# Kernel tuning notes

Hardware: AMD Instinct MI355X
Metric: run time of the kernel (lower is better)

The kernel has to match this reference:

```python
import jax, jax.numpy as jnp
import numpy as np

SEQ, B, I, H = 2048, 64, 512, 512


def setup_inputs() -> dict:
    key = jax.random.key(0)
    ks = jax.random.split(key, 5)
    s = 1.0 / np.sqrt(H)  # torch.nn.RNN init scale
    return {
        "x": jax.random.normal(ks[0], (SEQ, B, I), dtype=jnp.float32),
        "W_ih": jax.random.normal(ks[1], (H, I), dtype=jnp.float32) * s,
        "W_hh": jax.random.normal(ks[2], (H, H), dtype=jnp.float32) * s,
        "b_ih": jax.random.normal(ks[3], (H,), dtype=jnp.float32) * s,
        "b_hh": jax.random.normal(ks[4], (H,), dtype=jnp.float32) * s,
    }


def reference(x, W_ih, W_hh, b_ih, b_hh):
    # Precompute input projection for all timesteps in one big GEMM: [T,B,H]
    xw = jnp.einsum("tbi,hi->tbh", x, W_ih) + b_ih + b_hh

    def step(h, xt):
        # h: [B,H]; xt: [B,H] (already includes x_t W_ih^T + biases)
        h = jnp.tanh(xt + h @ W_hh.T)
        return h, h

    h0 = jnp.zeros((x.shape[1], W_hh.shape[0]), dtype=x.dtype)
    _, out = jax.lax.scan(step, h0, xw)  # out: [T,B,H]
    return out.reshape(-1, W_hh.shape[0])  # [T*B, H], matches out.view(-1, hidden)
```

## Files before the change

### kernel.cpp

```cpp
#include <hip/hip_runtime.h>
#include <cmath>


#define SEQ_T 2048
#define BATCH 64
#define KDIM 512
#define HDIM 512

typedef __fp16 h2v __attribute__((ext_vector_type(2)));
typedef __fp16 f16x8 __attribute__((ext_vector_type(8)));
typedef float f32x4 __attribute__((ext_vector_type(4)));

static __device__ __forceinline__ f16x8 pk8(float4 a, float4 b) {
  h2v p0 = __builtin_amdgcn_cvt_pkrtz(a.x, a.y);
  h2v p1 = __builtin_amdgcn_cvt_pkrtz(a.z, a.w);
  h2v p2 = __builtin_amdgcn_cvt_pkrtz(b.x, b.y);
  h2v p3 = __builtin_amdgcn_cvt_pkrtz(b.z, b.w);
  f16x8 r;
  r[0] = p0[0]; r[1] = p0[1]; r[2] = p1[0]; r[3] = p1[1];
  r[4] = p2[0]; r[5] = p2[1]; r[6] = p3[0]; r[7] = p3[1];
  return r;
}

#define G_LDA 72

#define MFM(mt, nt) \
  d##mt##nt = __builtin_amdgcn_mfma_f32_16x16x32_f16(fa##mt, fb##nt, d##mt##nt, 0, 0, 0);

#define EPI(mt, nt, bb)                                                     \
  {                                                                         \
    int row = m0 + wm + mt * 16 + (l >> 4) * 4;                             \
    int col = n0 + wn + nt * 16 + (l & 15);                                 \
    out[(size_t)(row + 0) * HDIM + col] = d##mt##nt[0] + bb;                \
    out[(size_t)(row + 1) * HDIM + col] = d##mt##nt[1] + bb;                \
    out[(size_t)(row + 2) * HDIM + col] = d##mt##nt[2] + bb;                \
    out[(size_t)(row + 3) * HDIM + col] = d##mt##nt[3] + bb;                \
  }

__global__ __launch_bounds__(256) void xw_gemm(const float* __restrict__ x,
                                               const float* __restrict__ Wih,
                                               const float* __restrict__ bih,
                                               const float* __restrict__ bhh,
                                               float* __restrict__ out) {
  __shared__ __fp16 At[128 * G_LDA];
  __shared__ __fp16 Bt[64 * G_LDA];
  const int tid = threadIdx.x;
  const int l = tid & 63;
  const int w = tid >> 6;
  const int m0 = (blockIdx.x >> 3) * 128;
  const int n0 = (blockIdx.x & 7) * 64;
  const int wm = (w >> 1) * 64;
  const int wn = (w & 1) * 32;

  const float bias0 = bih[n0 + wn + (l & 15)] + bhh[n0 + wn + (l & 15)];
  const float bias1 = bih[n0 + wn + 16 + (l & 15)] + bhh[n0 + wn + 16 + (l & 15)];

  f32x4 d00 = {0,0,0,0}, d01 = {0,0,0,0}, d10 = {0,0,0,0}, d11 = {0,0,0,0};
  f32x4 d20 = {0,0,0,0}, d21 = {0,0,0,0}, d30 = {0,0,0,0}, d31 = {0,0,0,0};

  for (int k0 = 0; k0 < KDIM; k0 += 64) {
    __syncthreads();
#pragma unroll
    for (int p = 0; p < 4; ++p) {
      int idx = tid + p * 256;
      int r = idx >> 3, sg = idx & 7;
      const float* ps = x + (size_t)(m0 + r) * KDIM + k0 + sg * 8;
      *(f16x8*)(At + r * G_LDA + sg * 8) =
          pk8(*(const float4*)ps, *(const float4*)(ps + 4));
    }
#pragma unroll
    for (int p = 0; p < 2; ++p) {
      int idx = tid + p * 256;
      int r = idx >> 3, sg = idx & 7;
      const float* ps = Wih + (size_t)(n0 + r) * KDIM + k0 + sg * 8;
      *(f16x8*)(Bt + r * G_LDA + sg * 8) =
          pk8(*(const float4*)ps, *(const float4*)(ps + 4));
    }
    __syncthreads();
#pragma unroll
    for (int kk = 0; kk < 2; ++kk) {
      const int kc = kk * 32 + (l >> 4) * 8;
      f16x8 fa0 = *(const f16x8*)(At + (wm + 0 * 16 + (l & 15)) * G_LDA + kc);
      f16x8 fa1 = *(const f16x8*)(At + (wm + 1 * 16 + (l & 15)) * G_LDA + kc);
      f16x8 fa2 = *(const f16x8*)(At + (wm + 2 * 16 + (l & 15)) * G_LDA + kc);
      f16x8 fa3 = *(const f16x8*)(At + (wm + 3 * 16 + (l & 15)) * G_LDA + kc);
      f16x8 fb0 = *(const f16x8*)(Bt + (wn + 0 * 16 + (l & 15)) * G_LDA + kc);
      f16x8 fb1 = *(const f16x8*)(Bt + (wn + 1 * 16 + (l & 15)) * G_LDA + kc);
      MFM(0, 0) MFM(1, 0) MFM(2, 0) MFM(3, 0)
      MFM(0, 1) MFM(1, 1) MFM(2, 1) MFM(3, 1)
    }
  }

  EPI(0, 0, bias0) EPI(1, 0, bias0) EPI(2, 0, bias0) EPI(3, 0, bias0)
  EPI(0, 1, bias1) EPI(1, 1, bias1) EPI(2, 1, bias1) EPI(3, 1, bias1)
}


#define REPB(M, c) M(c,0) M(c,1) M(c,2) M(c,3) M(c,4) M(c,5) \
                   M(c,6) M(c,7) M(c,8) M(c,9) M(c,10) M(c,11)

#define DECLB(c, n) f16x8 bf##c##_##n;
#define LOADB(c, n)                                        \
  {                                                        \
    const float* p = wr##c + 32 * n;                       \
    bf##c##_##n = pk8(*(const float4*)p, *(const float4*)(p + 4)); \
  }
#define PINB(c, n) asm volatile("" : "+a"(bf##c##_##n));
#define STOREB(c, n)                                                        \
  {                                                                         \
    const float* p = wr##c + 32 * n;                                        \
    *(f16x8*)(ldsm + (((n) - 12) * 4 + c) * 8192 + (tid << 4)) =            \
        pk8(*(const float4*)p, *(const float4*)(p + 4));                    \
  }

#define MF(c, n) \
  d##c = __builtin_amdgcn_mfma_f32_16x16x32_f16(acur, bf##c##_##n, d##c, 0, 0, 0);
#define MFL(c, n)                                                              \
  {                                                                            \
    f16x8 bl = *(const f16x8*)(ldsm + (((n) - 12) * 4 + c) * 8192 + (tid << 4)); \
    d##c = __builtin_amdgcn_mfma_f32_16x16x32_f16(acur, bl, d##c, 0, 0, 0);    \
  }

#define CH(n, nn)                                                \
  {                                                              \
    f16x8 anx = *(const f16x8*)(hcv + 64 * (nn) + goff);         \
    MF(0, n) MF(1, n) MF(2, n) MF(3, n)                          \
    acur = anx;                                                  \
  }
#define CHL(n, nn)                                               \
  {                                                              \
    f16x8 anx = *(const f16x8*)(hcv + 64 * (nn) + goff);         \
    MFL(0, n) MFL(1, n) MFL(2, n) MFL(3, n)                      \
    acur = anx;                                                  \
  }

#define WLDS_BYTES (16 * 8192)
#define HBUF0 WLDS_BYTES
#define LDS_TOTAL (WLDS_BYTES + 3 * 1024)

#define BAR()                                              \
  asm volatile("s_waitcnt lgkmcnt(0)" ::: "memory");       \
  __builtin_amdgcn_sched_barrier(0);                       \
  __builtin_amdgcn_s_barrier();                            \
  __builtin_amdgcn_sched_barrier(0);

__global__ __attribute__((amdgpu_flat_work_group_size(512, 512),
                          amdgpu_waves_per_eu(2, 2)))
void rnn_scan(const float* __restrict__ Whh, float* __restrict__ io) {
  extern __shared__ __align__(16) char ldsm[];
  const int tid = threadIdx.x;
  const int b = blockIdx.x;
  const int l = tid & 63;
  const int w = tid >> 6;
  const int m16 = l & 15;
  const int gh = l >> 4;
  const int goff = gh << 4;
  const int rb = w << 6;
  const int jo = rb + l;

  const float* wr0 = Whh + (size_t)(rb + 0 + m16) * KDIM + 8 * gh;
  const float* wr1 = Whh + (size_t)(rb + 16 + m16) * KDIM + 8 * gh;
  const float* wr2 = Whh + (size_t)(rb + 32 + m16) * KDIM + 8 * gh;
  const float* wr3 = Whh + (size_t)(rb + 48 + m16) * KDIM + 8 * gh;

  REPB(DECLB, 0) REPB(DECLB, 1) REPB(DECLB, 2) REPB(DECLB, 3)
  REPB(LOADB, 0) REPB(LOADB, 1) REPB(LOADB, 2) REPB(LOADB, 3)
  REPB(PINB, 0)  REPB(PINB, 1)  REPB(PINB, 2)  REPB(PINB, 3)

  STOREB(0, 12) STOREB(1, 12) STOREB(2, 12) STOREB(3, 12)
  STOREB(0, 13) STOREB(1, 13) STOREB(2, 13) STOREB(3, 13)
  STOREB(0, 14) STOREB(1, 14) STOREB(2, 14) STOREB(3, 14)
  STOREB(0, 15) STOREB(1, 15) STOREB(2, 15) STOREB(3, 15)

  if (tid < 512) ((unsigned short*)(ldsm + HBUF0))[tid] = 0;
  __syncthreads();

  char* hcur = ldsm + HBUF0;
  char* hnxt = ldsm + HBUF0 + 1024;
  char* hthr = ldsm + HBUF0 + 2048;

  float* iorow = io + (size_t)b * HDIM;

  for (int t = 0; t < SEQ_T; ++t) {
    float uin = iorow[jo];

    const char* hcv = hcur;
    f16x8 acur = *(const f16x8*)(hcv + goff);

    f32x4 d0 = {0.f, 0.f, 0.f, 0.f};
    f32x4 d1 = {0.f, 0.f, 0.f, 0.f};
    f32x4 d2 = {0.f, 0.f, 0.f, 0.f};
    f32x4 d3 = {0.f, 0.f, 0.f, 0.f};

    CH(0, 1)  CH(1, 2)   CH(2, 3)   CH(3, 4)
    CH(4, 5)  CH(5, 6)   CH(6, 7)   CH(7, 8)
    CH(8, 9)  CH(9, 10)  CH(10, 11) CH(11, 12)
    CHL(12, 13) CHL(13, 14) CHL(14, 15) CHL(15, 15)

    float za = (l & 16) ? d1[0] : d0[0];
    float zb = (l & 16) ? d3[0] : d2[0];
    float zs = (l & 32) ? zb : za;

    float z = uin + zs;
    float e = __expf(2.0f * z);
    float hn = 1.0f - 2.0f * __builtin_amdgcn_rcpf(e + 1.0f);
    iorow[jo] = hn;
    *(__fp16*)(hnxt + 2 * jo) = (__fp16)hn;

    char* tmp = hcur;
    hcur = hnxt; hnxt = hthr; hthr = tmp;
    iorow += (size_t)BATCH * HDIM;
    BAR();
  }
}

extern "C" void kernel_launch(void* const* d_in, const int* in_sizes, int n_in,
                              void* d_out, int out_size, void* d_ws, size_t ws_size,
                              hipStream_t stream) {
  const float* x = (const float*)d_in[0];
  const float* Wih = (const float*)d_in[1];
  const float* Whh = (const float*)d_in[2];
  const float* bih = (const float*)d_in[3];
  const float* bhh = (const float*)d_in[4];
  float* out = (float*)d_out;

  (void)hipFuncSetAttribute((const void*)rnn_scan,
                            hipFuncAttributeMaxDynamicSharedMemorySize,
                            LDS_TOTAL);

  const int M = SEQ_T * BATCH;
  dim3 g1((M / 128) * (HDIM / 64));
  xw_gemm<<<g1, 256, 0, stream>>>(x, Wih, bih, bhh, out);

  rnn_scan<<<BATCH, 512, LDS_TOTAL, stream>>>(Whh, out);
}
```

Before: 3.560 ms.

## Drop AGPR pinning of recurrent weights, prepack part of W_hh into workspace

Removes the inline-asm constraint that forced the register-resident W_hh fragments into AGPRs. A new w_prep kernel pre-converts weight chunks 8-11 to fp16 fragment layout in the workspace, and the scan loads them directly instead of converting them itself. The custom barrier macro with an explicit lgkmcnt wait is replaced by __syncthreads. This gives the compiler freedom over register allocation in the serial recurrence loop, at the cost of an extra small kernel launch and a risk of VGPR spills or worse MFMA operand placement.

```diff
diff --git a/kernel.cpp b/kernel.cpp
--- a/kernel.cpp
+++ b/kernel.cpp
@@ -20,6 +20,16 @@
   r[0] = p0[0]; r[1] = p0[1]; r[2] = p1[0]; r[3] = p1[1];
   r[4] = p2[0]; r[5] = p2[1]; r[6] = p3[0]; r[7] = p3[1];
   return r;
+}
+
+__global__ __launch_bounds__(256) void w_prep(const float* __restrict__ Whh,
+                                              f16x8* __restrict__ ws) {
+  int v = blockIdx.x * 256 + threadIdx.x;
+  int l = v & 63, w = (v >> 6) & 7, c = (v >> 9) & 3, n = (v >> 11) + 8;
+  int row = 64 * w + 16 * c + (l & 15);
+  int col = 32 * n + 8 * (l >> 4);
+  const float* p = Whh + (size_t)row * KDIM + col;
+  ws[v] = pk8(*(const float4*)p, *(const float4*)(p + 4));
 }
 
 #define G_LDA 72
@@ -96,8 +106,8 @@
 }
 
 
-#define REPB(M, c) M(c,0) M(c,1) M(c,2) M(c,3) M(c,4) M(c,5) \
-                   M(c,6) M(c,7) M(c,8) M(c,9) M(c,10) M(c,11)
+#define REPB(M, c) M(c,0) M(c,1) M(c,2) M(c,3) M(c,4) M(c,5) M(c,6) M(c,7)
+#define REPW(M, c) M(c,8) M(c,9) M(c,10) M(c,11)
 
 #define DECLB(c, n) f16x8 bf##c##_##n;
 #define LOADB(c, n)                                        \
@@ -105,7 +115,7 @@
     const float* p = wr##c + 32 * n;                       \
     bf##c##_##n = pk8(*(const float4*)p, *(const float4*)(p + 4)); \
   }
-#define PINB(c, n) asm volatile("" : "+a"(bf##c##_##n));
+#define LOADW(c, n) bf##c##_##n = wsp[(((n) - 8) * 4 + (c)) * 512];
 #define STOREB(c, n)                                                        \
   {                                                                         \
     const float* p = wr##c + 32 * n;                                        \
@@ -138,15 +148,10 @@
 #define HBUF0 WLDS_BYTES
 #define LDS_TOTAL (WLDS_BYTES + 3 * 1024)
 
-#define BAR()                                              \
-  asm volatile("s_waitcnt lgkmcnt(0)" ::: "memory");       \
-  __builtin_amdgcn_sched_barrier(0);                       \
-  __builtin_amdgcn_s_barrier();                            \
-  __builtin_amdgcn_sched_barrier(0);
-
 __global__ __attribute__((amdgpu_flat_work_group_size(512, 512),
                           amdgpu_waves_per_eu(2, 2)))
-void rnn_scan(const float* __restrict__ Whh, float* __restrict__ io) {
+void rnn_scan(const float* __restrict__ Whh, const f16x8* __restrict__ ws,
+              float* __restrict__ io) {
   extern __shared__ __align__(16) char ldsm[];
   const int tid = threadIdx.x;
   const int b = blockIdx.x;
@@ -162,10 +167,12 @@
   const float* wr1 = Whh + (size_t)(rb + 16 + m16) * KDIM + 8 * gh;
   const float* wr2 = Whh + (size_t)(rb + 32 + m16) * KDIM + 8 * gh;
   const float* wr3 = Whh + (size_t)(rb + 48 + m16) * KDIM + 8 * gh;
+  const f16x8* wsp = ws + (w * 64 + l);
 
   REPB(DECLB, 0) REPB(DECLB, 1) REPB(DECLB, 2) REPB(DECLB, 3)
+  REPW(DECLB, 0) REPW(DECLB, 1) REPW(DECLB, 2) REPW(DECLB, 3)
   REPB(LOADB, 0) REPB(LOADB, 1) REPB(LOADB, 2) REPB(LOADB, 3)
-  REPB(PINB, 0)  REPB(PINB, 1)  REPB(PINB, 2)  REPB(PINB, 3)
+  REPW(LOADW, 0) REPW(LOADW, 1) REPW(LOADW, 2) REPW(LOADW, 3)
 
   STOREB(0, 12) STOREB(1, 12) STOREB(2, 12) STOREB(3, 12)
   STOREB(0, 13) STOREB(1, 13) STOREB(2, 13) STOREB(3, 13)
@@ -210,7 +217,7 @@
     char* tmp = hcur;
     hcur = hnxt; hnxt = hthr; hthr = tmp;
     iorow += (size_t)BATCH * HDIM;
-    BAR();
+    __syncthreads();
   }
 }
 
@@ -223,14 +230,17 @@
   const float* bih = (const float*)d_in[3];
   const float* bhh = (const float*)d_in[4];
   float* out = (float*)d_out;
+  f16x8* ws = (f16x8*)d_ws;
 
   (void)hipFuncSetAttribute((const void*)rnn_scan,
                             hipFuncAttributeMaxDynamicSharedMemorySize,
                             LDS_TOTAL);
 
+  w_prep<<<32, 256, 0, stream>>>(Whh, ws);
+
   const int M = SEQ_T * BATCH;
   dim3 g1((M / 128) * (HDIM / 64));
   xw_gemm<<<g1, 256, 0, stream>>>(x, Wih, bih, bhh, out);
 
-  rnn_scan<<<BATCH, 512, LDS_TOTAL, stream>>>(Whh, out);
-}
+  rnn_scan<<<BATCH, 512, LDS_TOTAL, stream>>>(Whh, ws, out);
+}
```

Measured after the change: 3.361 ms. 1.06x faster.
